# Kernel optimization log

Hardware: AMD Instinct MI355X
Metric: run time of the kernel (lower is better)

The kernel has to match this reference:

```python
import jax, jax.numpy as jnp
import numpy as np

HEAD_DIM = 128
ROPE_THETA = 10000.0


def _rope_cos_sin(positions, head_dim, theta):
    # positions: [T] int -> cos/sin [T, head_dim] (LLaMA half-split convention)
    inv_freq = 1.0 / (theta ** (jnp.arange(0, head_dim, 2, dtype=jnp.float32) / head_dim))
    ang = positions.astype(jnp.float32)[:, None] * inv_freq  # [T, D/2]
    cos = jnp.concatenate([jnp.cos(ang), jnp.cos(ang)], axis=-1)
    sin = jnp.concatenate([jnp.sin(ang), jnp.sin(ang)], axis=-1)
    return cos, sin


def _apply_rope(x, cos, sin):
    # x: [T, H, D]; rotate_half: (-x2, x1)
    half = x.shape[-1] // 2
    rot = jnp.concatenate([-x[..., half:], x[..., :half]], axis=-1)
    return x * cos[:, None, :] + rot * sin[:, None, :]


def setup_inputs() -> dict:
    key = jax.random.key(0)
    ks = jax.random.split(key, 5)
    T, hid = 4096, 4096
    S = 1024  # equal-length sequences -> B = T // S = 4
    Hq, Hk, D = 32, 8, HEAD_DIM
    hidden = jax.random.normal(ks[0], (T, hid), dtype=jnp.float32)
    positions = (jnp.arange(T, dtype=jnp.int32) % S)
    q_w = jax.random.normal(ks[1], (Hq * D, hid), dtype=jnp.float32) * 0.02
    k_w = jax.random.normal(ks[2], (Hk * D, hid), dtype=jnp.float32) * 0.02
    v_w = jax.random.normal(ks[3], (Hk * D, hid), dtype=jnp.float32) * 0.02
    o_w = jax.random.normal(ks[4], (hid, Hq * D), dtype=jnp.float32) * 0.02
    return {"hidden": hidden, "positions": positions, "q_w": q_w, "k_w": k_w,
            "v_w": v_w, "o_w": o_w, "seq_len": S}


def reference(hidden, positions, q_w, k_w, v_w, o_w, seq_len):
    T, hid = hidden.shape
    D = HEAD_DIM
    Hq = q_w.shape[0] // D
    Hk = k_w.shape[0] // D
    G = Hq // Hk  # num_kv_groups
    S = int(seq_len)
    B = T // S
    # QKV projections (ColumnParallel, tp=1): y = x @ W^T
    q = (hidden @ q_w.T).reshape(T, Hq, D)
    k = (hidden @ k_w.T).reshape(T, Hk, D)
    v = (hidden @ v_w.T).reshape(T, Hk, D)
    # fused RoPE on q and k
    cos, sin = _rope_cos_sin(positions, D, ROPE_THETA)
    q = _apply_rope(q, cos, sin)
    k = _apply_rope(k, cos, sin)
    # varlen (equal-length) causal GQA attention
    q = q.reshape(B, S, Hk, G, D)
    k = k.reshape(B, S, Hk, D)
    v = v.reshape(B, S, Hk, D)
    scale = 1.0 / np.sqrt(D).astype(np.float32)
    scores = jnp.einsum('bqhgd,bkhd->bhgqk', q, k) * scale  # [B,Hk,G,S,S]
    causal = jnp.tril(jnp.ones((S, S), dtype=bool))
    scores = jnp.where(causal, scores, jnp.asarray(-1e30, scores.dtype))
    attn = jax.nn.softmax(scores, axis=-1)
    out = jnp.einsum('bhgqk,bkhd->bqhgd', attn, v).reshape(T, Hq * D)
    # output projection (RowParallel, tp=1)
    return out @ o_w.T
```

## Files before the change

kernel.cpp:

```cpp
#include <hip/hip_runtime.h>
#include <hip/hip_bf16.h>

typedef __attribute__((ext_vector_type(8))) short bf16x8;
typedef __attribute__((ext_vector_type(4))) float f32x4;
typedef __attribute__((ext_vector_type(8))) unsigned short u16x8;

__device__ inline unsigned short f2bf(float f) {
  unsigned u = __builtin_bit_cast(unsigned, f);
  u += 0x7FFFu + ((u >> 16) & 1u);
  return (unsigned short)(u >> 16);
}
__device__ inline float b2f(unsigned short h) {
  unsigned u = ((unsigned)h) << 16;
  return __builtin_bit_cast(float, u);
}

typedef const __attribute__((address_space(1))) void* gas_ptr;
typedef __attribute__((address_space(3))) void* las_ptr;
__device__ inline void load_lds16(const void* g, void* l) {
  __builtin_amdgcn_global_load_lds((gas_ptr)g, (las_ptr)l, 16, 0, 0);
}

#define PHB() do { asm volatile("" ::: "memory"); __builtin_amdgcn_s_barrier(); \
                   __builtin_amdgcn_sched_barrier(0); } while (0)

__global__ __launch_bounds__(256) void cvt_f32_bf16(const float* __restrict__ src,
                                                    unsigned short* __restrict__ dst,
                                                    int n4) {
  int i = blockIdx.x * 256 + threadIdx.x;
  if (i >= n4) return;
  float4 v = ((const float4*)src)[i];
  ushort4 o;
  o.x = f2bf(v.x); o.y = f2bf(v.y); o.z = f2bf(v.z); o.w = f2bf(v.w);
  ((ushort4*)dst)[i] = o;
}

template <int NLOADS>
__device__ inline void stage_tile(const unsigned short* __restrict__ g, int ld,
                                  size_t grow0, int kcol0, char* ldsdst, int tid) {
#pragma unroll
  for (int i = 0; i < NLOADS; ++i) {
    int c = tid + i * 512;
    int r = c >> 3;
    int k = (c & 7) ^ (r & 7);
    load_lds16(g + (grow0 + r) * ld + kcol0 + k * 8, ldsdst + c * 16);
  }
}

template <int Kc, int Nc, bool OUT_F32>
__global__ __launch_bounds__(512, 1) void gemmT(const unsigned short* __restrict__ A,
                                                const unsigned short* __restrict__ B,
                                                void* __restrict__ Cv) {
  __shared__ __attribute__((aligned(16))) char lds[147456];
  const int tid = threadIdx.x;
  const int wave = tid >> 6, lane = tid & 63;
  const int l15 = lane & 15, l4 = lane >> 4;
  const int wr = wave >> 2, wc = wave & 3;
  const int nTN = Nc >> 8;
  const int cpx = gridDim.x >> 3;
  const int orig = blockIdx.x;
  const int wg = (orig & 7) * cpx + (orig >> 3);
  const int bm = wg / nTN, bn = wg % nTN;
  const size_t rowA0 = (size_t)bm << 7, rowB0 = (size_t)bn << 8;
  const int nt = Kc >> 6;

  stage_tile<2>(A, Kc, rowA0, 0,  lds + 0,             tid);
  stage_tile<4>(B, Kc, rowB0, 0,  lds + 16384,         tid);
  stage_tile<2>(A, Kc, rowA0, 64, lds + 49152,         tid);
  stage_tile<4>(B, Kc, rowB0, 64, lds + 49152 + 16384, tid);
  asm volatile("s_waitcnt vmcnt(6)" ::: "memory");
  __builtin_amdgcn_s_barrier();
  __builtin_amdgcn_sched_barrier(0);

  f32x4 acc[4][4] = {};

#pragma unroll 3
  for (int t = 0; t < nt; ++t) {
    char* cbuf = lds + (t % 3) * 49152;
    char* sbuf = lds + ((t + 2) % 3) * 49152;
    const char* bufA = cbuf;
    const char* bufB = cbuf + 16384;
    const int kc2 = (t + 2) << 6;

    bf16x8 af[4][2], bf[4][2];

#pragma unroll
    for (int m = 0; m < 4; ++m) {
      int row = wr * 64 + m * 16 + l15;
#pragma unroll
      for (int kk = 0; kk < 2; ++kk)
        af[m][kk] = *(const bf16x8*)(bufA + (row << 7) + (((kk * 4 + l4) ^ (row & 7)) << 4));
    }
#pragma unroll
    for (int n = 0; n < 2; ++n) {
      int row = wc * 64 + n * 16 + l15;
#pragma unroll
      for (int kk = 0; kk < 2; ++kk)
        bf[n][kk] = *(const bf16x8*)(bufB + (row << 7) + (((kk * 4 + l4) ^ (row & 7)) << 4));
    }
    if (t < nt - 2) stage_tile<4>(B, Kc, rowB0, kc2, sbuf + 16384, tid);
    __builtin_amdgcn_s_barrier();
    asm volatile("s_waitcnt lgkmcnt(0)" ::: "memory");
    __builtin_amdgcn_sched_barrier(0);
    __builtin_amdgcn_s_setprio(1);
#pragma unroll
    for (int m = 0; m < 4; ++m)
#pragma unroll
      for (int n = 0; n < 2; ++n)
#pragma unroll
        for (int kk = 0; kk < 2; ++kk)
          acc[m][n] = __builtin_amdgcn_mfma_f32_16x16x32_bf16(af[m][kk], bf[n][kk], acc[m][n], 0, 0, 0);
    __builtin_amdgcn_s_setprio(0);
    PHB();

#pragma unroll
    for (int n = 2; n < 4; ++n) {
      int row = wc * 64 + n * 16 + l15;
#pragma unroll
      for (int kk = 0; kk < 2; ++kk)
        bf[n][kk] = *(const bf16x8*)(bufB + (row << 7) + (((kk * 4 + l4) ^ (row & 7)) << 4));
    }
    if (t < nt - 2) stage_tile<2>(A, Kc, rowA0, kc2, sbuf, tid);
    if (t <= nt - 3) { asm volatile("s_waitcnt vmcnt(6)" ::: "memory"); }
    else             { asm volatile("s_waitcnt vmcnt(0)" ::: "memory"); }
    __builtin_amdgcn_s_barrier();
    asm volatile("s_waitcnt lgkmcnt(0)" ::: "memory");
    __builtin_amdgcn_sched_barrier(0);
    __builtin_amdgcn_s_setprio(1);
#pragma unroll
    for (int m = 0; m < 4; ++m)
#pragma unroll
      for (int n = 2; n < 4; ++n)
#pragma unroll
        for (int kk = 0; kk < 2; ++kk)
          acc[m][n] = __builtin_amdgcn_mfma_f32_16x16x32_bf16(af[m][kk], bf[n][kk], acc[m][n], 0, 0, 0);
    __builtin_amdgcn_s_setprio(0);
    PHB();
  }

#pragma unroll
  for (int m = 0; m < 4; ++m)
#pragma unroll
    for (int n = 0; n < 4; ++n)
#pragma unroll
      for (int r = 0; r < 4; ++r) {
        size_t row = rowA0 + wr * 64 + m * 16 + l4 * 4 + r;
        size_t col = rowB0 + wc * 64 + n * 16 + l15;
        float v = acc[m][n][r];
        if (OUT_F32) ((float*)Cv)[row * Nc + col] = v;
        else         ((unsigned short*)Cv)[row * Nc + col] = f2bf(v);
      }
}

__global__ __launch_bounds__(256) void rope_kernel(unsigned short* __restrict__ qkv,
                                                   const int* __restrict__ positions) {
  int gw = (blockIdx.x * 256 + threadIdx.x) >> 6;
  int lane = threadIdx.x & 63;
  int t = gw / 40, h = gw % 40;
  size_t col0 = (h < 32) ? ((size_t)h << 7) : (4096 + ((size_t)(h - 32) << 7));
  unsigned short* p = qkv + (size_t)t * 6144 + col0;
  float pos = (float)positions[t];
  float inv = powf(10000.0f, -(float)lane * (1.0f / 64.0f));
  float ang = pos * inv;
  float s, c;
  sincosf(ang, &s, &c);
  float x1 = b2f(p[lane]);
  float x2 = b2f(p[lane + 64]);
  p[lane]      = f2bf(x1 * c - x2 * s);
  p[lane + 64] = f2bf(x2 * c + x1 * s);
}

__global__ __launch_bounds__(256, 4) void attn_kernel(const unsigned short* __restrict__ qkv,
                                                      unsigned short* __restrict__ ao) {
  int orig = blockIdx.x;
  int wgid = (orig & 7) * 128 + (orig >> 3);
  int pair = wgid & 7;
  int hq = (wgid >> 3) & 31;
  int b  = wgid >> 8;
  int hk = hq >> 2;
  int tid = threadIdx.x, wave = tid >> 6, lane = tid & 63;
  int l15 = lane & 15, l4 = lane >> 4;

  __shared__ __attribute__((aligned(16))) char ldsA[16384];
  __shared__ __attribute__((aligned(16))) unsigned short Vt[128][72];
  unsigned short (*Ks)[128]    = (unsigned short (*)[128])ldsA;
  unsigned short (*Ps)[16][72] = (unsigned short (*)[16][72])ldsA;

  const float scale = 0.08838834764831845f;

#pragma unroll 1
  for (int iq = 0; iq < 2; ++iq) {
    const int qa = iq ? (15 - pair) : pair;
    const size_t qrow0 = (size_t)(b * 1024 + qa * 64 + wave * 16);

    bf16x8 qf[4];
    {
      const unsigned short* qp = qkv + (qrow0 + l15) * 6144 + ((size_t)hq << 7) + l4 * 8;
#pragma unroll
      for (int kc = 0; kc < 4; ++kc) qf[kc] = *(const bf16x8*)(qp + kc * 32);
    }

    float m_i[4], l_i[4];
    f32x4 oacc[8];
#pragma unroll
    for (int r = 0; r < 4; ++r) { m_i[r] = -1e30f; l_i[r] = 0.0f; }
#pragma unroll
    for (int d = 0; d < 8; ++d) oacc[d] = f32x4{0.f, 0.f, 0.f, 0.f};

#pragma unroll 1
    for (int kt = 0; kt <= qa; ++kt) {
      __syncthreads();

      const unsigned short* kbase = qkv + (size_t)(b * 1024 + kt * 64) * 6144 + 4096 + ((size_t)hk << 7);
#pragma unroll
      for (int j = 0; j < 4; ++j) {
        int c = (j * 4 + wave) * 64 + lane;
        int r = c >> 4;
        int cc = (c & 15) ^ (r & 7);
        load_lds16(kbase + (size_t)r * 6144 + cc * 8, ldsA + c * 16);
      }
      {
        const unsigned short* vp = qkv + (size_t)(b * 1024 + kt * 64 + lane) * 6144 + 5120 + ((size_t)hk << 7) + wave * 32;
        u16x8 va0 = *(const u16x8*)(vp);
        u16x8 va1 = *(const u16x8*)(vp + 8);
        u16x8 va2 = *(const u16x8*)(vp + 16);
        u16x8 va3 = *(const u16x8*)(vp + 24);
        int d0 = wave * 32;
#pragma unroll
        for (int c = 0; c < 8; ++c) Vt[d0 + c][lane]      = va0[c];
#pragma unroll
        for (int c = 0; c < 8; ++c) Vt[d0 + 8 + c][lane]  = va1[c];
#pragma unroll
        for (int c = 0; c < 8; ++c) Vt[d0 + 16 + c][lane] = va2[c];
#pragma unroll
        for (int c = 0; c < 8; ++c) Vt[d0 + 24 + c][lane] = va3[c];
      }
      __syncthreads();

      float pbuf[4][4];
      float tmax[4] = {-1e30f, -1e30f, -1e30f, -1e30f};
#pragma unroll
      for (int nt = 0; nt < 4; ++nt) {
        f32x4 sacc = {0.f, 0.f, 0.f, 0.f};
        int row = nt * 16 + l15;
#pragma unroll
        for (int kc = 0; kc < 4; ++kc) {
          const unsigned short* kp = &Ks[0][0] + row * 128 + (((kc * 4 + l4) ^ (row & 7)) * 8);
          bf16x8 kf = *(const bf16x8*)kp;
          sacc = __builtin_amdgcn_mfma_f32_16x16x32_bf16(qf[kc], kf, sacc, 0, 0, 0);
        }
#pragma unroll
        for (int r = 0; r < 4; ++r) {
          float s = sacc[r] * scale;
          if (kt == qa) {
            int kcol = nt * 16 + l15;
            int qrow = wave * 16 + l4 * 4 + r;
            if (kcol > qrow) s = -1e30f;
          }
          pbuf[nt][r] = s;
          tmax[r] = fmaxf(tmax[r], s);
        }
      }
      __syncthreads();

#pragma unroll
      for (int r = 0; r < 4; ++r) {
        float v = tmax[r];
        v = fmaxf(v, __shfl_xor(v, 1));
        v = fmaxf(v, __shfl_xor(v, 2));
        v = fmaxf(v, __shfl_xor(v, 4));
        v = fmaxf(v, __shfl_xor(v, 8));
        tmax[r] = v;
      }
      float rescale[4];
#pragma unroll
      for (int r = 0; r < 4; ++r) {
        float mn = fmaxf(m_i[r], tmax[r]);
        rescale[r] = __expf(m_i[r] - mn);
        m_i[r] = mn;
      }
      float psum[4] = {0.f, 0.f, 0.f, 0.f};
#pragma unroll
      for (int nt = 0; nt < 4; ++nt)
#pragma unroll
        for (int r = 0; r < 4; ++r) {
          float p = __expf(pbuf[nt][r] - m_i[r]);
          pbuf[nt][r] = p;
          psum[r] += p;
        }
#pragma unroll
      for (int r = 0; r < 4; ++r) {
        float v = psum[r];
        v += __shfl_xor(v, 1);
        v += __shfl_xor(v, 2);
        v += __shfl_xor(v, 4);
        v += __shfl_xor(v, 8);
        l_i[r] = l_i[r] * rescale[r] + v;
      }
#pragma unroll
      for (int d = 0; d < 8; ++d)
#pragma unroll
        for (int r = 0; r < 4; ++r) oacc[d][r] *= rescale[r];

#pragma unroll
      for (int nt = 0; nt < 4; ++nt)
#pragma unroll
        for (int r = 0; r < 4; ++r)
          Ps[wave][l4 * 4 + r][nt * 16 + l15] = f2bf(pbuf[nt][r]);

#pragma unroll
      for (int h = 0; h < 2; ++h) {
        bf16x8 pa = *(const bf16x8*)&Ps[wave][l15][h * 32 + l4 * 8];
#pragma unroll
        for (int d = 0; d < 8; ++d) {
          bf16x8 vf = *(const bf16x8*)&Vt[d * 16 + l15][h * 32 + l4 * 8];
          oacc[d] = __builtin_amdgcn_mfma_f32_16x16x32_bf16(pa, vf, oacc[d], 0, 0, 0);
        }
      }
    }

#pragma unroll
    for (int d = 0; d < 8; ++d)
#pragma unroll
      for (int r = 0; r < 4; ++r) {
        size_t row = qrow0 + l4 * 4 + r;
        size_t col = ((size_t)hq << 7) + d * 16 + l15;
        ao[row * 4096 + col] = f2bf(oacc[d][r] / l_i[r]);
      }
  }
}

extern "C" void kernel_launch(void* const* d_in, const int* in_sizes, int n_in,
                              void* d_out, int out_size, void* d_ws, size_t ws_size,
                              hipStream_t stream) {
  const float* hidden    = (const float*)d_in[0];
  const int*   positions = (const int*)d_in[1];
  const float* q_w       = (const float*)d_in[2];
  const float* k_w       = (const float*)d_in[3];
  const float* v_w       = (const float*)d_in[4];
  const float* o_w       = (const float*)d_in[5];
  float* out = (float*)d_out;

  char* ws = (char*)d_ws;
  unsigned short* hidB  = (unsigned short*)(ws);
  unsigned short* wqkvB = (unsigned short*)(ws + 33554432);
  unsigned short* woB   = (unsigned short*)(ws + 83886080);
  unsigned short* qkvB  = (unsigned short*)(ws + 117440512);
  unsigned short* aoB   = (unsigned short*)(ws + 167772160);

  cvt_f32_bf16<<<16384, 256, 0, stream>>>(hidden, hidB, 4194304);
  cvt_f32_bf16<<<16384, 256, 0, stream>>>(q_w, wqkvB, 4194304);
  cvt_f32_bf16<<<4096, 256, 0, stream>>>(k_w, wqkvB + 16777216, 1048576);
  cvt_f32_bf16<<<4096, 256, 0, stream>>>(v_w, wqkvB + 20971520, 1048576);
  cvt_f32_bf16<<<16384, 256, 0, stream>>>(o_w, woB, 4194304);

  gemmT<4096, 6144, false><<<768, 512, 0, stream>>>(hidB, wqkvB, (void*)qkvB);

  rope_kernel<<<40960, 256, 0, stream>>>(qkvB, positions);

  attn_kernel<<<1024, 256, 0, stream>>>(qkvB, aoB);

  gemmT<4096, 4096, true><<<512, 512, 0, stream>>>(aoB, woB, (void*)out);
}
```

Baseline: 559.1 us.

## Swizzle attention LDS tiles, split P buffer, add MFMA priority, 2D XCD GEMM mapping

The attention kernel now gives K, transposed V and P their own LDS arrays. This removes the aliasing that forced a barrier between the score computation and the P writes. V transpose and P stores use XOR-swizzled columns instead of padded rows, to cut LDS bank conflicts. MFMA loops are wrapped in s_setprio raises, and the GEMM tile-to-XCD assignment now places each XCD on a 2D block of the output for better L2 reuse. Separate buffers raise LDS use per workgroup, which may affect occupancy.

```diff
diff --git a/kernel.cpp b/kernel.cpp
--- a/kernel.cpp
+++ b/kernel.cpp
@@ -47,7 +47,15 @@
   }
 }
 
-template <int Kc, int Nc, bool OUT_F32>
+__device__ inline void xcd_decode(int orig, int nTM, int nTN, int& bm, int& bn) {
+  int x = orig & 7, i = orig >> 3;
+  int xr = x >> 1, xc = x & 1;
+  int bmch = nTM >> 2, bnch = nTN >> 1;
+  bm = xr * bmch + i / bnch;
+  bn = xc * bnch + i % bnch;
+}
+
+template <int Kc, int Nc, int Mc, bool OUT_F32>
 __global__ __launch_bounds__(512, 1) void gemmT(const unsigned short* __restrict__ A,
                                                 const unsigned short* __restrict__ B,
                                                 void* __restrict__ Cv) {
@@ -56,11 +64,8 @@
   const int wave = tid >> 6, lane = tid & 63;
   const int l15 = lane & 15, l4 = lane >> 4;
   const int wr = wave >> 2, wc = wave & 3;
-  const int nTN = Nc >> 8;
-  const int cpx = gridDim.x >> 3;
-  const int orig = blockIdx.x;
-  const int wg = (orig & 7) * cpx + (orig >> 3);
-  const int bm = wg / nTN, bn = wg % nTN;
+  int bm, bn;
+  xcd_decode(blockIdx.x, Mc >> 7, Nc >> 8, bm, bn);
   const size_t rowA0 = (size_t)bm << 7, rowB0 = (size_t)bn << 8;
   const int nt = Kc >> 6;
 
@@ -181,10 +186,9 @@
   int tid = threadIdx.x, wave = tid >> 6, lane = tid & 63;
   int l15 = lane & 15, l4 = lane >> 4;
 
-  __shared__ __attribute__((aligned(16))) char ldsA[16384];
-  __shared__ __attribute__((aligned(16))) unsigned short Vt[128][72];
-  unsigned short (*Ks)[128]    = (unsigned short (*)[128])ldsA;
-  unsigned short (*Ps)[16][72] = (unsigned short (*)[16][72])ldsA;
+  __shared__ __attribute__((aligned(16))) unsigned short Ks[64][128];
+  __shared__ __attribute__((aligned(16))) unsigned short Vt[128][64];
+  __shared__ __attribute__((aligned(16))) unsigned short Ps[4][16][64];
 
   const float scale = 0.08838834764831845f;
 
@@ -217,7 +221,7 @@
         int c = (j * 4 + wave) * 64 + lane;
         int r = c >> 4;
         int cc = (c & 15) ^ (r & 7);
-        load_lds16(kbase + (size_t)r * 6144 + cc * 8, ldsA + c * 16);
+        load_lds16(kbase + (size_t)r * 6144 + cc * 8, (char*)&Ks[0][0] + c * 16);
       }
       {
         const unsigned short* vp = qkv + (size_t)(b * 1024 + kt * 64 + lane) * 6144 + 5120 + ((size_t)hk << 7) + wave * 32;
@@ -227,13 +231,13 @@
         u16x8 va3 = *(const u16x8*)(vp + 24);
         int d0 = wave * 32;
 #pragma unroll
-        for (int c = 0; c < 8; ++c) Vt[d0 + c][lane]      = va0[c];
-#pragma unroll
-        for (int c = 0; c < 8; ++c) Vt[d0 + 8 + c][lane]  = va1[c];
-#pragma unroll
-        for (int c = 0; c < 8; ++c) Vt[d0 + 16 + c][lane] = va2[c];
-#pragma unroll
-        for (int c = 0; c < 8; ++c) Vt[d0 + 24 + c][lane] = va3[c];
+        for (int c = 0; c < 8; ++c) {
+          int sc = lane ^ ((c & 7) << 3);
+          Vt[d0 + c][sc]      = va0[c];
+          Vt[d0 + 8 + c][sc]  = va1[c];
+          Vt[d0 + 16 + c][sc] = va2[c];
+          Vt[d0 + 24 + c][sc] = va3[c];
+        }
       }
       __syncthreads();
 
@@ -243,12 +247,14 @@
       for (int nt = 0; nt < 4; ++nt) {
         f32x4 sacc = {0.f, 0.f, 0.f, 0.f};
         int row = nt * 16 + l15;
+        __builtin_amdgcn_s_setprio(1);
 #pragma unroll
         for (int kc = 0; kc < 4; ++kc) {
           const unsigned short* kp = &Ks[0][0] + row * 128 + (((kc * 4 + l4) ^ (row & 7)) * 8);
           bf16x8 kf = *(const bf16x8*)kp;
           sacc = __builtin_amdgcn_mfma_f32_16x16x32_bf16(qf[kc], kf, sacc, 0, 0, 0);
         }
+        __builtin_amdgcn_s_setprio(0);
 #pragma unroll
         for (int r = 0; r < 4; ++r) {
           float s = sacc[r] * scale;
@@ -261,7 +267,6 @@
           tmax[r] = fmaxf(tmax[r], s);
         }
       }
-      __syncthreads();
 
 #pragma unroll
       for (int r = 0; r < 4; ++r) {
@@ -305,17 +310,22 @@
 #pragma unroll
       for (int nt = 0; nt < 4; ++nt)
 #pragma unroll
-        for (int r = 0; r < 4; ++r)
-          Ps[wave][l4 * 4 + r][nt * 16 + l15] = f2bf(pbuf[nt][r]);
+        for (int r = 0; r < 4; ++r) {
+          int r4 = l4 * 4 + r;
+          Ps[wave][r4][(nt * 16 + l15) ^ ((r4 & 7) << 3)] = f2bf(pbuf[nt][r]);
+        }
 
 #pragma unroll
       for (int h = 0; h < 2; ++h) {
-        bf16x8 pa = *(const bf16x8*)&Ps[wave][l15][h * 32 + l4 * 8];
+        bf16x8 pa = *(const bf16x8*)(&Ps[wave][0][0] + l15 * 64 + ((h * 32 + l4 * 8) ^ ((l15 & 7) << 3)));
+        __builtin_amdgcn_s_setprio(1);
 #pragma unroll
         for (int d = 0; d < 8; ++d) {
-          bf16x8 vf = *(const bf16x8*)&Vt[d * 16 + l15][h * 32 + l4 * 8];
+          int row = d * 16 + l15;
+          bf16x8 vf = *(const bf16x8*)(&Vt[0][0] + row * 64 + ((h * 32 + l4 * 8) ^ ((row & 7) << 3)));
           oacc[d] = __builtin_amdgcn_mfma_f32_16x16x32_bf16(pa, vf, oacc[d], 0, 0, 0);
         }
+        __builtin_amdgcn_s_setprio(0);
       }
     }
 
@@ -354,11 +364,11 @@
   cvt_f32_bf16<<<4096, 256, 0, stream>>>(v_w, wqkvB + 20971520, 1048576);
   cvt_f32_bf16<<<16384, 256, 0, stream>>>(o_w, woB, 4194304);
 
-  gemmT<4096, 6144, false><<<768, 512, 0, stream>>>(hidB, wqkvB, (void*)qkvB);
+  gemmT<4096, 6144, 4096, false><<<768, 512, 0, stream>>>(hidB, wqkvB, (void*)qkvB);
 
   rope_kernel<<<40960, 256, 0, stream>>>(qkvB, positions);
 
   attn_kernel<<<1024, 256, 0, stream>>>(qkvB, aoB);
 
-  gemmT<4096, 4096, true><<<512, 512, 0, stream>>>(aoB, woB, (void*)out);
-}
+  gemmT<4096, 4096, 4096, true><<<512, 512, 0, stream>>>(aoB, woB, (void*)out);
+}
```

Result: no change. 549.3 us (-1.8%).
